# Kernel optimization log

Hardware: AMD Instinct MI355X
Metric: run time of the kernel (lower is better)

The kernel has to match this reference:

```python
import jax, jax.numpy as jnp
import numpy as np
import math

S, B, HID = 1024, 2, 2048
NH, KVH, HDIM = 16, 4, 128
FFN, E, TOPK = 4096, 8, 2
CAP_F = 1.0
Q_PER_KV = NH // KVH
GROUP = (Q_PER_KV + 2) * HDIM
QKV_SIZE = KVH * GROUP
T = S * B
CAPACITY = max(4, int(math.ceil(TOPK * CAP_F * T / E)))
EPS = 1.1920929e-07


def _xavier(key, shape, fan_in, fan_out):
    lim = math.sqrt(6.0 / (fan_in + fan_out))
    return jax.random.uniform(key, shape, jnp.float32, -lim, lim)


def setup_inputs() -> dict:
    key = jax.random.key(0)
    ks = jax.random.split(key, 8)
    return {
        'hidden_states': jax.random.normal(ks[0], (S, B, HID), jnp.float32),
        'ln1_w': jnp.ones((HID,), jnp.float32),
        'ln1_b': jnp.zeros((HID,), jnp.float32),
        'qkv_w': _xavier(ks[1], (QKV_SIZE, HID), HID, QKV_SIZE),
        'proj_w': _xavier(ks[2], (HID, NH * HDIM), NH * HDIM, HID),
        'ln2_w': jnp.ones((HID,), jnp.float32),
        'ln2_b': jnp.zeros((HID,), jnp.float32),
        'gate_w': _xavier(ks[3], (HID, E), HID, E),
        'w1': _xavier(ks[4], (E, HID, FFN), HID, FFN),  # expert fc1 [E, HID, FFN]
        'w2': _xavier(ks[5], (E, FFN, HID), FFN, HID),  # expert fc2 [E, FFN, HID]
    }


def _layer_norm(x, w, b):
    mu = x.mean(-1, keepdims=True)
    var = ((x - mu) ** 2).mean(-1, keepdims=True)
    return (x - mu) * jax.lax.rsqrt(var + 1e-5) * w + b


def _attention(hs, ln1_w, ln1_b, qkv_w, proj_w):
    ln1 = _layer_norm(hs, ln1_w, ln1_b)
    qkv = jnp.einsum('sbh,oh->sbo', ln1, qkv_w)
    qkv = qkv.reshape(S, B, KVH, GROUP)
    q_dim = Q_PER_KV * HDIM
    q = qkv[..., :q_dim].reshape(S, B, NH, HDIM)
    k = qkv[..., q_dim:q_dim + HDIM]          # [S,B,KVH,HDIM]
    v = qkv[..., q_dim + HDIM:]               # [S,B,KVH,HDIM]
    # batch-first, GQA expand kv heads
    q_bf = q.transpose(1, 0, 2, 3)                         # [B,S,NH,HDIM]
    k_bf = jnp.repeat(k.transpose(1, 0, 2, 3), Q_PER_KV, axis=2)
    v_bf = jnp.repeat(v.transpose(1, 0, 2, 3), Q_PER_KV, axis=2)
    scale = 1.0 / math.sqrt(HDIM)
    scores = jnp.einsum('bqhd,bkhd->bhqk', q_bf, k_bf) * scale
    causal = jnp.tril(jnp.ones((S, S), bool))
    scores = jnp.where(causal, scores, jnp.finfo(scores.dtype).min)
    attn = jax.nn.softmax(scores, axis=-1)
    out = jnp.einsum('bhqk,bkhd->bqhd', attn, v_bf)        # [B,S,NH,HDIM]
    out_sp = out.transpose(1, 0, 2, 3).reshape(S, B, NH * HDIM)
    return jnp.einsum('sbo,ho->sbh', out_sp, proj_w)


def _moe(x, gate_w, w1, w2):
    # x: [T, HID]; deterministic DeepSpeed-style top-2 gating with capacity drop
    logits = jnp.einsum('th,he->te', x, gate_w)
    gates = jax.nn.softmax(logits, axis=-1)
    idx1 = jnp.argmax(gates, axis=-1)
    mask1 = jax.nn.one_hot(idx1, E, dtype=jnp.int32)
    logits2 = jnp.where(mask1.astype(bool), jnp.finfo(logits.dtype).min, logits)
    idx2 = jnp.argmax(logits2, axis=-1)
    mask2 = jax.nn.one_hot(idx2, E, dtype=jnp.int32)
    loc1 = jnp.cumsum(mask1, axis=0) - mask1                 # position within expert
    loc2 = jnp.cumsum(mask2, axis=0) - mask2 + mask1.sum(axis=0, keepdims=True)
    mask1 = mask1 * (loc1 < CAPACITY)
    mask2 = mask2 * (loc2 < CAPACITY)
    m1f = mask1.astype(gates.dtype)
    m2f = mask2.astype(gates.dtype)
    g1 = (gates * m1f).sum(-1)
    g2 = (gates * m2f).sum(-1)
    denom = jnp.maximum(g1 + g2, EPS)
    g1, g2 = g1 / denom, g2 / denom
    p1 = (loc1 * mask1).sum(-1)
    p2 = (loc2 * mask2).sum(-1)
    c1 = (g1[:, None] * m1f)[:, :, None] * jax.nn.one_hot(p1, CAPACITY, dtype=gates.dtype)[:, None, :]
    c2 = (g2[:, None] * m2f)[:, :, None] * jax.nn.one_hot(p2, CAPACITY, dtype=gates.dtype)[:, None, :]
    combine = c1 + c2                                        # [T,E,C]
    dispatch = (combine > 0).astype(x.dtype)
    xe = jnp.einsum('tec,th->ech', dispatch, x)              # [E,C,HID]
    h = jax.nn.gelu(jnp.einsum('ech,ehf->ecf', xe, w1), approximate=False)
    eo = jnp.einsum('ecf,efh->ech', h, w2)                   # [E,C,HID]
    return jnp.einsum('tec,ech->th', combine, eo)


def reference(hidden_states, ln1_w, ln1_b, qkv_w, proj_w, ln2_w, ln2_b, gate_w, w1, w2):
    h1 = hidden_states + _attention(hidden_states, ln1_w, ln1_b, qkv_w, proj_w)
    ln2 = _layer_norm(h1, ln2_w, ln2_b)
    moe_out = _moe(ln2.reshape(T, HID), gate_w, w1, w2).reshape(S, B, HID)
    return h1 + moe_out
```

## Files before the change

### kernel.cpp

```cpp
#include <hip/hip_runtime.h>
#include <math.h>

#define S_LEN 1024
#define BATCH 2
#define HIDN  2048
#define NHEAD 16
#define KVHN  4
#define HDIM  128
#define FFND  4096
#define NEXP  8
#define CAPC  512
#define TTOK  2048
#define QKVSZ 3072
#define GRP   768

#define BM  128
#define BKS 32
#define BKM 64
#define LDT 40

typedef float           f32x4 __attribute__((ext_vector_type(4)));
typedef __bf16          bf16x8 __attribute__((ext_vector_type(8)));
typedef unsigned short  u16x8 __attribute__((ext_vector_type(8)));
typedef unsigned short  u16x4 __attribute__((ext_vector_type(4)));

static __device__ __forceinline__ unsigned short f2bf(float f) {
  unsigned int u = __builtin_bit_cast(unsigned int, f);
  u += 0x7FFFu + ((u >> 16) & 1u);
  return (unsigned short)(u >> 16);
}
static __device__ __forceinline__ float bf2f(unsigned short h) {
  unsigned int u = ((unsigned int)h) << 16;
  return __builtin_bit_cast(float, u);
}
static __device__ __forceinline__ bf16x8 ldbf8(const unsigned short* p) {
  return __builtin_bit_cast(bf16x8, *(const u16x8*)p);
}
static __device__ __forceinline__ f32x4 mfma16(bf16x8 a, bf16x8 b, f32x4 c) {
  return __builtin_amdgcn_mfma_f32_16x16x32_bf16(a, b, c, 0, 0, 0);
}
static __device__ __forceinline__ void gl_lds16(const unsigned short* g, unsigned short* l) {
  __builtin_amdgcn_global_load_lds(
      (const __attribute__((address_space(1))) unsigned int*)g,
      (__attribute__((address_space(3))) unsigned int*)l, 16, 0, 0);
}

__global__ __launch_bounds__(256) void ln_kernel(
    const float* __restrict__ X, const float* __restrict__ W, const float* __restrict__ Bi,
    unsigned short* __restrict__ Yh, unsigned short* __restrict__ Yl, float* __restrict__ Yf) {
  __shared__ float red[256];
  int t = blockIdx.x, tid = threadIdx.x;
  const float* row = X + (size_t)t * HIDN;
  float x[8];
  {
    float4 a = *(const float4*)(row + tid * 8);
    float4 b = *(const float4*)(row + tid * 8 + 4);
    x[0]=a.x; x[1]=a.y; x[2]=a.z; x[3]=a.w; x[4]=b.x; x[5]=b.y; x[6]=b.z; x[7]=b.w;
  }
  float s = 0.f;
#pragma unroll
  for (int j = 0; j < 8; j++) s += x[j];
  red[tid] = s; __syncthreads();
  for (int o = 128; o > 0; o >>= 1) { if (tid < o) red[tid] += red[tid + o]; __syncthreads(); }
  float mu = red[0] * (1.0f / HIDN);
  __syncthreads();
  float ss = 0.f;
#pragma unroll
  for (int j = 0; j < 8; j++) { float d = x[j] - mu; ss += d * d; }
  red[tid] = ss; __syncthreads();
  for (int o = 128; o > 0; o >>= 1) { if (tid < o) red[tid] += red[tid + o]; __syncthreads(); }
  float var = red[0] * (1.0f / HIDN);
  float rstd = 1.0f / sqrtf(var + 1e-5f);
#pragma unroll
  for (int j = 0; j < 8; j++) {
    int hh = tid * 8 + j;
    float y = (x[j] - mu) * rstd * W[hh] + Bi[hh];
    size_t idx = (size_t)t * HIDN + hh;
    if (Yf) Yf[idx] = y;
    unsigned short hv = f2bf(y);
    Yh[idx] = hv;
    if (Yl) Yl[idx] = f2bf(y - bf2f(hv));
  }
}

__global__ __launch_bounds__(256) void wsplit(const float* __restrict__ W,
    unsigned short* __restrict__ Wh, unsigned short* __restrict__ Wl) {
  size_t i = ((size_t)blockIdx.x * 256 + threadIdx.x) * 8;
  float4 a = *(const float4*)(W + i);
  float4 b = *(const float4*)(W + i + 4);
  float v[8] = {a.x, a.y, a.z, a.w, b.x, b.y, b.z, b.w};
  u16x8 hv, lv;
#pragma unroll
  for (int j = 0; j < 8; j++) {
    unsigned short h = f2bf(v[j]);
    hv[j] = h; lv[j] = f2bf(v[j] - bf2f(h));
  }
  *(u16x8*)(Wh + i) = hv;
  *(u16x8*)(Wl + i) = lv;
}

__global__ __launch_bounds__(256) void tconv(const float* __restrict__ W,
    unsigned short* __restrict__ Wt, int K, int N) {
  __shared__ unsigned short T[64][72];
  int z = blockIdx.z;
  const float* Wz = W + (size_t)z * K * N;
  unsigned short* Oz = Wt + (size_t)z * N * K;
  int k0 = blockIdx.y * 64, n0 = blockIdx.x * 64;
  int tid = threadIdx.x;
  int kr = (tid >> 4) << 1, n4 = (tid & 15) << 2;
#pragma unroll
  for (int i = 0; i < 2; i++) {
    int k = kr + i * 32;
    float4 a = *(const float4*)(Wz + (size_t)(k0 + k) * N + n0 + n4);
    float4 b = *(const float4*)(Wz + (size_t)(k0 + k + 1) * N + n0 + n4);
    float av[4] = {a.x, a.y, a.z, a.w};
    float bv[4] = {b.x, b.y, b.z, b.w};
#pragma unroll
    for (int j = 0; j < 4; j++) {
      unsigned int pk = (unsigned int)f2bf(av[j]) | ((unsigned int)f2bf(bv[j]) << 16);
      *(unsigned int*)&T[n4 + j][k] = pk;
    }
  }
  __syncthreads();
  int nr = tid >> 3, c = (tid & 7) << 3;
#pragma unroll
  for (int r = 0; r < 2; r++) {
    int n = nr + r * 32;
    u16x8 v = *(const u16x8*)&T[n][c];
    *(u16x8*)(Oz + (size_t)(n0 + n) * K + k0 + c) = v;
  }
}

__global__ __launch_bounds__(256) void gemm_x3s(
    const unsigned short* __restrict__ Ah, const unsigned short* __restrict__ Al,
    const unsigned short* __restrict__ Bh, const unsigned short* __restrict__ Bl,
    float* __restrict__ Cp, int M, int N, int K2, int ldk) {
  __shared__ __align__(16) unsigned short sAh[2][4096], sAl[2][4096], sBh[2][4096], sBl[2][4096];
  int tid = threadIdx.x;
  int nbm = M >> 7, nbn = N >> 7, per = nbm * nbn;
  int cpx = gridDim.x >> 3;
  int bid = blockIdx.x;
  int l = (bid & 7) * cpx + (bid >> 3);
  int kh = l / per;
  int r = l % per;
  int nb = r / nbm, mb = r % nbm;
  int m0 = mb * BM, n0 = nb * BM;
  size_t ko = (size_t)kh * K2;
  int wv = tid >> 6, lane = tid & 63;
  int wr = wv >> 1, wc = wv & 1;
  int lm = lane & 15, lk = lane >> 4;
  f32x4 acc[4][4];
#pragma unroll
  for (int mi = 0; mi < 4; mi++)
#pragma unroll
    for (int ni = 0; ni < 4; ni++) { acc[mi][ni][0]=0.f; acc[mi][ni][1]=0.f; acc[mi][ni][2]=0.f; acc[mi][ni][3]=0.f; }
  int ri = lane >> 2, ccx = lane & 3;
  int swze = (ccx ^ (ri & 3)) * 8;
  int g0 = wv * 2, g1 = g0 + 1;
  const unsigned short* pah0 = Ah + (size_t)(m0 + g0 * 16 + ri) * ldk + ko + swze;
  const unsigned short* pah1 = Ah + (size_t)(m0 + g1 * 16 + ri) * ldk + ko + swze;
  const unsigned short* pal0 = Al + (size_t)(m0 + g0 * 16 + ri) * ldk + ko + swze;
  const unsigned short* pal1 = Al + (size_t)(m0 + g1 * 16 + ri) * ldk + ko + swze;
  const unsigned short* pbh0 = Bh + (size_t)(n0 + g0 * 16 + ri) * ldk + ko + swze;
  const unsigned short* pbh1 = Bh + (size_t)(n0 + g1 * 16 + ri) * ldk + ko + swze;
  const unsigned short* pbl0 = Bl + (size_t)(n0 + g0 * 16 + ri) * ldk + ko + swze;
  const unsigned short* pbl1 = Bl + (size_t)(n0 + g1 * 16 + ri) * ldk + ko + swze;
  int d0 = g0 * 512, d1 = g1 * 512;
  auto stage = [&](int buf, int ks) {
    gl_lds16(pah0 + ks, &sAh[buf][d0]); gl_lds16(pah1 + ks, &sAh[buf][d1]);
    gl_lds16(pal0 + ks, &sAl[buf][d0]); gl_lds16(pal1 + ks, &sAl[buf][d1]);
    gl_lds16(pbh0 + ks, &sBh[buf][d0]); gl_lds16(pbh1 + ks, &sBh[buf][d1]);
    gl_lds16(pbl0 + ks, &sBl[buf][d0]); gl_lds16(pbl1 + ks, &sBl[buf][d1]);
  };
  int nt = K2 / BKS;
  stage(0, 0);
  stage(1, BKS);
  int sa = (lk ^ (lm & 3)) * 8;
  for (int t = 0; t < nt; t++) {
    if (t + 1 < nt) { asm volatile("s_waitcnt vmcnt(8)" ::: "memory"); }
    else            { asm volatile("s_waitcnt vmcnt(0)" ::: "memory"); }
    __builtin_amdgcn_sched_barrier(0);
    __builtin_amdgcn_s_barrier();
    int cur = t & 1;
    bf16x8 fah[4], fal[4], fbh[4], fbl[4];
#pragma unroll
    for (int mi = 0; mi < 4; mi++) {
      int ro = (wr * 64 + mi * 16 + lm) * 32 + sa;
      fah[mi] = ldbf8(&sAh[cur][ro]); fal[mi] = ldbf8(&sAl[cur][ro]);
    }
#pragma unroll
    for (int ni = 0; ni < 4; ni++) {
      int ro = (wc * 64 + ni * 16 + lm) * 32 + sa;
      fbh[ni] = ldbf8(&sBh[cur][ro]); fbl[ni] = ldbf8(&sBl[cur][ro]);
    }
#pragma unroll
    for (int mi = 0; mi < 4; mi++)
#pragma unroll
      for (int ni = 0; ni < 4; ni++) {
        acc[mi][ni] = mfma16(fah[mi], fbh[ni], acc[mi][ni]);
        acc[mi][ni] = mfma16(fal[mi], fbh[ni], acc[mi][ni]);
        acc[mi][ni] = mfma16(fah[mi], fbl[ni], acc[mi][ni]);
      }
    __builtin_amdgcn_s_barrier();
    if (t + 2 < nt) stage(cur, (t + 2) * BKS);
  }
  float* Cslab = Cp + (size_t)kh * M * N;
#pragma unroll
  for (int mi = 0; mi < 4; mi++)
#pragma unroll
    for (int ni = 0; ni < 4; ni++)
#pragma unroll
      for (int rr = 0; rr < 4; rr++) {
        int row = m0 + wr * 64 + mi * 16 + lk * 4 + rr;
        int col = n0 + wc * 64 + ni * 16 + lm;
        Cslab[(size_t)row * N + col] = acc[mi][ni][rr];
      }
}

template<int GELU, int SPLITK>
__global__ __launch_bounds__(256) void gemm_moe(
    const unsigned short* __restrict__ A, const unsigned short* __restrict__ Bt,
    void* __restrict__ Cp, int M, int N, int K, int ld) {
  __shared__ __align__(16) unsigned short sA[2][8192], sB[2][8192];
  int tid = threadIdx.x;
  int nbm = M >> 7, nbn = N >> 7, per = nbm * nbn;
  int cpx = gridDim.x >> 3;
  int bid = blockIdx.x;
  int l = (bid & 7) * cpx + (bid >> 3);
  int z = l / per;
  int r = l % per;
  int nb = r / nbm, mb = r % nbm;
  int m0 = mb * BM, n0 = nb * BM;
  const unsigned short* Az;
  const unsigned short* Bz;
  if (SPLITK) {
    int e = z >> 1, kh = z & 1;
    Az = A + (size_t)e * M * ld + (size_t)kh * K;
    Bz = Bt + (size_t)e * N * ld + (size_t)kh * K;
  } else {
    Az = A + (size_t)z * M * ld;
    Bz = Bt + (size_t)z * N * ld;
  }
  int wv = tid >> 6, lane = tid & 63;
  int wr = wv >> 1, wc = wv & 1;
  int lm = lane & 15, lk = lane >> 4;
  f32x4 acc[4][4];
#pragma unroll
  for (int mi = 0; mi < 4; mi++)
#pragma unroll
    for (int ni = 0; ni < 4; ni++) { acc[mi][ni][0]=0.f; acc[mi][ni][1]=0.f; acc[mi][ni][2]=0.f; acc[mi][ni][3]=0.f; }
  int ri = lane >> 3, cc8 = lane & 7;
  int swze = (cc8 ^ ri) * 8;
  const unsigned short* pa[4];
  const unsigned short* pb[4];
#pragma unroll
  for (int j = 0; j < 4; j++) {
    int g = wv * 4 + j;
    pa[j] = Az + (size_t)(m0 + g * 8 + ri) * ld + swze;
    pb[j] = Bz + (size_t)(n0 + g * 8 + ri) * ld + swze;
  }
  int dbase = wv * 4 * 512;
  auto stage = [&](int buf, int ks) {
#pragma unroll
    for (int j = 0; j < 4; j++) {
      gl_lds16(pa[j] + ks, &sA[buf][dbase + j * 512]);
      gl_lds16(pb[j] + ks, &sB[buf][dbase + j * 512]);
    }
  };
  int nt = K / BKM;
  stage(0, 0);
  stage(1, BKM);
  int sw = lm & 7;
  for (int t = 0; t < nt; t++) {
    if (t + 1 < nt) { asm volatile("s_waitcnt vmcnt(8)" ::: "memory"); }
    else            { asm volatile("s_waitcnt vmcnt(0)" ::: "memory"); }
    __builtin_amdgcn_sched_barrier(0);
    __builtin_amdgcn_s_barrier();
    int cur = t & 1;
#pragma unroll
    for (int h = 0; h < 2; h++) {
      int kc = lk + h * 4;
      int sa = ((kc ^ sw)) * 8;
      bf16x8 fa[4], fb[4];
#pragma unroll
      for (int mi = 0; mi < 4; mi++) fa[mi] = ldbf8(&sA[cur][(wr * 64 + mi * 16 + lm) * 64 + sa]);
#pragma unroll
      for (int ni = 0; ni < 4; ni++) fb[ni] = ldbf8(&sB[cur][(wc * 64 + ni * 16 + lm) * 64 + sa]);
#pragma unroll
      for (int mi = 0; mi < 4; mi++)
#pragma unroll
        for (int ni = 0; ni < 4; ni++)
          acc[mi][ni] = mfma16(fa[mi], fb[ni], acc[mi][ni]);
    }
    __builtin_amdgcn_s_barrier();
    if (t + 2 < nt) stage(cur, (t + 2) * BKM);
  }
#pragma unroll
  for (int mi = 0; mi < 4; mi++)
#pragma unroll
    for (int ni = 0; ni < 4; ni++)
#pragma unroll
      for (int rr = 0; rr < 4; rr++) {
        int row = m0 + wr * 64 + mi * 16 + lk * 4 + rr;
        int col = n0 + wc * 64 + ni * 16 + lm;
        size_t idx = (size_t)z * M * N + (size_t)row * N + col;
        float v = acc[mi][ni][rr];
        if (GELU) {
          float gv = 0.5f * v * (1.0f + erff(v * 0.70710678118654752f));
          ((unsigned short*)Cp)[idx] = f2bf(gv);
        } else {
          ((float*)Cp)[idx] = v;
        }
      }
}

__global__ __launch_bounds__(256) void h1comb(
    const float* __restrict__ hs, const float* __restrict__ p, float* __restrict__ h1) {
  size_t i = ((size_t)blockIdx.x * 256 + threadIdx.x) * 8;
  const float* p0 = p + i;
  const float* p1 = p + (size_t)TTOK * HIDN + i;
#pragma unroll
  for (int j = 0; j < 8; j += 4) {
    float4 a = *(const float4*)(hs + i + j);
    float4 b = *(const float4*)(p0 + j);
    float4 c = *(const float4*)(p1 + j);
    float4 o;
    o.x = a.x + b.x + c.x; o.y = a.y + b.y + c.y;
    o.z = a.z + b.z + c.z; o.w = a.w + b.w + c.w;
    *(float4*)(h1 + i + j) = o;
  }
}

__global__ __launch_bounds__(256) void repack_kernel(
    const float* __restrict__ qkvp,
    unsigned short* __restrict__ Qh, unsigned short* __restrict__ Ql,
    unsigned short* __restrict__ Kh, unsigned short* __restrict__ Kl,
    unsigned short* __restrict__ Vh, unsigned short* __restrict__ Vl) {
  int t = blockIdx.x; int s = t / BATCH, b = t % BATCH;
  const float* row0 = qkvp + (size_t)t * QKVSZ;
  const float* row1 = row0 + (size_t)TTOK * QKVSZ;
  int tid = threadIdx.x;
  for (int idx = tid; idx < 2048; idx += 256) {
    int hh = idx >> 7, d = idx & 127;
    int o_in = (hh >> 2) * GRP + (hh & 3) * 128 + d;
    float val = row0[o_in] + row1[o_in];
    unsigned short hv = f2bf(val), lv = f2bf(val - bf2f(hv));
    size_t o = ((size_t)(b * NHEAD + hh) * S_LEN + s) * HDIM + d;
    Qh[o] = hv; Ql[o] = lv;
  }
  for (int idx = tid; idx < 512; idx += 256) {
    int g = idx >> 7, d = idx & 127;
    int o_in = g * GRP + 512 + d;
    float val = row0[o_in] + row1[o_in];
    unsigned short hv = f2bf(val), lv = f2bf(val - bf2f(hv));
    size_t o = ((size_t)(b * KVHN + g) * S_LEN + s) * HDIM + d;
    Kh[o] = hv; Kl[o] = lv;
  }
  for (int idx = tid; idx < 512; idx += 256) {
    int g = idx >> 7, d = idx & 127;
    int o_in = g * GRP + 640 + d;
    float val = row0[o_in] + row1[o_in];
    unsigned short hv = f2bf(val), lv = f2bf(val - bf2f(hv));
    size_t o = ((size_t)(b * KVHN + g) * HDIM + d) * S_LEN + s;
    Vh[o] = hv; Vl[o] = lv;
  }
}

__global__ __launch_bounds__(256) void attn4(
    const unsigned short* __restrict__ Qh, const unsigned short* __restrict__ Ql,
    const unsigned short* __restrict__ Kh, const unsigned short* __restrict__ Kl,
    const unsigned short* __restrict__ Vh, const unsigned short* __restrict__ Vl,
    unsigned short* __restrict__ Oh, unsigned short* __restrict__ Ol) {
  __shared__ __align__(16) unsigned short sK[2][2][32 * 128];
  __shared__ __align__(16) unsigned short Ph[4][2][16 * LDT], Pl[4][2][16 * LDT];
  int qt = blockIdx.x, g = blockIdx.y, b = blockIdx.z;
  int tid = threadIdx.x, wv = tid >> 6, lane = tid & 63;
  int lm = lane & 15, lk = lane >> 4;
  int hh = g * 4 + wv;
  int q0 = qt * 16;
  const float scale = 0.08838834764831845f;
  int r0 = wv * 4 + (lane >> 4);
  int c16 = lane & 15;
  int dsw = (c16 * 8) ^ ((r0 & 7) << 3);
  const unsigned short* kbh = Kh + (size_t)((b * KVHN + g) * S_LEN) * HDIM;
  const unsigned short* kbl = Kl + (size_t)((b * KVHN + g) * S_LEN) * HDIM;
  auto stageK = [&](int buf, int k0) {
    unsigned short* dh = &sK[buf][0][0];
    unsigned short* dl = &sK[buf][1][0];
    gl_lds16(kbh + (size_t)(k0 + r0) * HDIM + dsw,      dh + wv * 512);
    gl_lds16(kbh + (size_t)(k0 + r0 + 16) * HDIM + dsw, dh + 2048 + wv * 512);
    gl_lds16(kbl + (size_t)(k0 + r0) * HDIM + dsw,      dl + wv * 512);
    gl_lds16(kbl + (size_t)(k0 + r0 + 16) * HDIM + dsw, dl + 2048 + wv * 512);
  };
  bf16x8 qfh[4], qfl[4];
  {
    size_t qb = ((size_t)(b * NHEAD + hh) * S_LEN + q0 + lm) * HDIM + lk * 8;
#pragma unroll
    for (int dc = 0; dc < 4; dc++) {
      qfh[dc] = ldbf8(Qh + qb + dc * 32);
      qfl[dc] = ldbf8(Ql + qb + dc * 32);
    }
  }
  f32x4 accO[8];
#pragma unroll
  for (int dt = 0; dt < 8; dt++) { accO[dt][0]=0.f; accO[dt][1]=0.f; accO[dt][2]=0.f; accO[dt][3]=0.f; }
  float mrun = -3.4e38f, lrun = 0.f;
  int nch = (q0 + 47) >> 5;
  stageK(0, 0);
  asm volatile("s_waitcnt vmcnt(0)" ::: "memory");
  __syncthreads();
  int cur = 0;
  for (int ck = 0; ck < nch; ck++) {
    int k0 = ck * 32;
    if (ck + 1 < nch) stageK(cur ^ 1, k0 + 32);
    f32x4 sc[2];
    sc[0][0]=0.f; sc[0][1]=0.f; sc[0][2]=0.f; sc[0][3]=0.f;
    sc[1][0]=0.f; sc[1][1]=0.f; sc[1][2]=0.f; sc[1][3]=0.f;
#pragma unroll
    for (int t2 = 0; t2 < 2; t2++) {
      int row = t2 * 16 + lm;
#pragma unroll
      for (int dc = 0; dc < 4; dc++) {
        int ce = (dc * 32 + lk * 8) ^ ((row & 7) << 3);
        bf16x8 kfh = ldbf8(&sK[cur][0][row * 128 + ce]);
        bf16x8 kfl = ldbf8(&sK[cur][1][row * 128 + ce]);
        sc[t2] = mfma16(kfh, qfh[dc], sc[t2]);
        sc[t2] = mfma16(kfl, qfh[dc], sc[t2]);
        sc[t2] = mfma16(kfh, qfl[dc], sc[t2]);
      }
    }
    float pv[8];
    float pmax = -3.4e38f;
#pragma unroll
    for (int t2 = 0; t2 < 2; t2++)
#pragma unroll
      for (int rr = 0; rr < 4; rr++) {
        int key = k0 + t2 * 16 + lk * 4 + rr;
        float sv = sc[t2][rr] * scale;
        if (key > q0 + lm) sv = -3.4e38f;
        pv[t2 * 4 + rr] = sv;
        pmax = fmaxf(pmax, sv);
      }
    pmax = fmaxf(pmax, __shfl_xor(pmax, 16));
    pmax = fmaxf(pmax, __shfl_xor(pmax, 32));
    float mnew = fmaxf(mrun, pmax);
    float fsc = expf(mrun - mnew);
    float psum = 0.f;
#pragma unroll
    for (int j = 0; j < 8; j++) { pv[j] = expf(pv[j] - mnew); psum += pv[j]; }
    psum = psum + __shfl_xor(psum, 16);
    psum = psum + __shfl_xor(psum, 32);
    lrun = lrun * fsc + psum;
#pragma unroll
    for (int dt = 0; dt < 8; dt++)
#pragma unroll
      for (int rr = 0; rr < 4; rr++) accO[dt][rr] *= fsc;
    int pb = ck & 1;
#pragma unroll
    for (int t2 = 0; t2 < 2; t2++) {
      u16x4 wh, wl;
#pragma unroll
      for (int rr = 0; rr < 4; rr++) {
        float p = pv[t2 * 4 + rr];
        unsigned short hv = f2bf(p);
        wh[rr] = hv; wl[rr] = f2bf(p - bf2f(hv));
      }
      int ad = lm * LDT + t2 * 16 + lk * 4;
      *(u16x4*)&Ph[wv][pb][ad] = wh;
      *(u16x4*)&Pl[wv][pb][ad] = wl;
    }
    bf16x8 pfh = ldbf8(&Ph[wv][pb][lm * LDT + lk * 8]);
    bf16x8 pfl = ldbf8(&Pl[wv][pb][lm * LDT + lk * 8]);
#pragma unroll
    for (int dt = 0; dt < 8; dt++) {
      size_t vo = ((size_t)((b * KVHN + g) * HDIM + dt * 16 + lm)) * S_LEN + k0 + lk * 8;
      bf16x8 vfh = ldbf8(Vh + vo);
      bf16x8 vfl = ldbf8(Vl + vo);
      accO[dt] = mfma16(vfh, pfh, accO[dt]);
      accO[dt] = mfma16(vfl, pfh, accO[dt]);
      accO[dt] = mfma16(vfh, pfl, accO[dt]);
    }
    mrun = mnew;
    asm volatile("s_waitcnt vmcnt(0)" ::: "memory");
    __syncthreads();
    cur ^= 1;
  }
  float inv = 1.0f / lrun;
#pragma unroll
  for (int dt = 0; dt < 8; dt++)
#pragma unroll
    for (int rr = 0; rr < 4; rr++) {
      float o = accO[dt][rr] * inv;
      int d = dt * 16 + lk * 4 + rr;
      int srow = q0 + lm;
      size_t idx = ((size_t)(srow * BATCH + b)) * HIDN + hh * HDIM + d;
      unsigned short hv = f2bf(o);
      Oh[idx] = hv; Ol[idx] = f2bf(o - bf2f(hv));
    }
}

__global__ __launch_bounds__(256) void gate_logits_kernel(
    const float* __restrict__ X, const float* __restrict__ GW, float* __restrict__ L) {
  __shared__ float red[256][8];
  int t = blockIdx.x, tid = threadIdx.x;
  const float* x = X + (size_t)t * HIDN + tid * 8;
  float acc[8] = {0.f,0.f,0.f,0.f,0.f,0.f,0.f,0.f};
#pragma unroll
  for (int j = 0; j < 8; j++) {
    float xv = x[j];
    const float* gp = GW + (size_t)(tid * 8 + j) * NEXP;
    float4 g0 = *(const float4*)gp;
    float4 g1 = *(const float4*)(gp + 4);
    acc[0] += xv * g0.x; acc[1] += xv * g0.y; acc[2] += xv * g0.z; acc[3] += xv * g0.w;
    acc[4] += xv * g1.x; acc[5] += xv * g1.y; acc[6] += xv * g1.z; acc[7] += xv * g1.w;
  }
#pragma unroll
  for (int k = 0; k < 8; k++) red[tid][k] = acc[k];
  __syncthreads();
  for (int o = 128; o > 0; o >>= 1) {
    if (tid < o) {
#pragma unroll
      for (int k = 0; k < 8; k++) red[tid][k] += red[tid + o][k];
    }
    __syncthreads();
  }
  if (tid < 8) L[(size_t)t * NEXP + tid] = red[0][tid];
}

__global__ __launch_bounds__(1024) void routing_kernel(
    const float* __restrict__ L, int* __restrict__ slot_token,
    int* __restrict__ tE1, int* __restrict__ tP1, float* __restrict__ tG1,
    int* __restrict__ tE2, int* __restrict__ tP2, float* __restrict__ tG2) {
  __shared__ unsigned int sc[1024][8];
  __shared__ unsigned int stot[8];
  int i = threadIdx.x;
  for (int j = i; j < NEXP * CAPC; j += 1024) slot_token[j] = -1;

  int e1[2], e2[2]; float g1[2], g2[2];
  unsigned int v[8] = {0,0,0,0,0,0,0,0};
#pragma unroll
  for (int u = 0; u < 2; u++) {
    int t = 2 * i + u;
    float l[8];
    float m = -3.4e38f;
#pragma unroll
    for (int e = 0; e < 8; e++) { l[e] = L[(size_t)t * NEXP + e]; m = fmaxf(m, l[e]); }
    float ex[8]; float se = 0.f;
#pragma unroll
    for (int e = 0; e < 8; e++) { ex[e] = expf(l[e] - m); se += ex[e]; }
    int b1 = 0; float bv = l[0];
    for (int e = 1; e < 8; e++) if (l[e] > bv) { bv = l[e]; b1 = e; }
    int b2 = -1; float bv2 = 0.f;
    for (int e = 0; e < 8; e++) {
      if (e == b1) continue;
      if (b2 < 0 || l[e] > bv2) { b2 = e; bv2 = l[e]; }
    }
    e1[u] = b1; e2[u] = b2;
    g1[u] = ex[b1] / se; g2[u] = ex[b2] / se;
    v[b1 >> 1] += 1u << ((b1 & 1) * 16);
    v[4 + (b2 >> 1)] += 1u << ((b2 & 1) * 16);
  }
  unsigned int cur[8];
#pragma unroll
  for (int k = 0; k < 8; k++) cur[k] = v[k];
  for (int off = 1; off < 1024; off <<= 1) {
#pragma unroll
    for (int k = 0; k < 8; k++) sc[i][k] = cur[k];
    __syncthreads();
    if (i >= off) {
#pragma unroll
      for (int k = 0; k < 8; k++) cur[k] += sc[i - off][k];
    }
    __syncthreads();
  }
  if (i == 1023) {
#pragma unroll
    for (int k = 0; k < 8; k++) stot[k] = cur[k];
  }
  __syncthreads();
  unsigned int excl[8];
#pragma unroll
  for (int k = 0; k < 8; k++) excl[k] = cur[k] - v[k];

#pragma unroll
  for (int u = 0; u < 2; u++) {
    int t = 2 * i + u;
    int a1 = e1[u], a2 = e2[u];
    int loc1 = (int)((excl[a1 >> 1] >> ((a1 & 1) * 16)) & 0xFFFFu);
    int loc2 = (int)((excl[4 + (a2 >> 1)] >> ((a2 & 1) * 16)) & 0xFFFFu);
    if (u == 1) {
      if (a1 == e1[0]) loc1 += 1;
      if (a2 == e2[0]) loc2 += 1;
    }
    loc2 += (int)((stot[a2 >> 1] >> ((a2 & 1) * 16)) & 0xFFFFu);
    bool k1 = loc1 < CAPC, k2 = loc2 < CAPC;
    float G1 = k1 ? g1[u] : 0.f, G2 = k2 ? g2[u] : 0.f;
    float den = fmaxf(G1 + G2, 1.1920929e-07f);
    G1 /= den; G2 /= den;
    tE1[t] = a1; tP1[t] = k1 ? loc1 : 0; tG1[t] = G1;
    tE2[t] = a2; tP2[t] = k2 ? loc2 : 0; tG2[t] = G2;
    if (k1) slot_token[a1 * CAPC + loc1] = t;
    if (k2) slot_token[a2 * CAPC + loc2] = t;
  }
}

__global__ __launch_bounds__(256) void gather_kernel(
    const int* __restrict__ slot_token, const unsigned short* __restrict__ Xb,
    unsigned short* __restrict__ XE) {
  int slot = blockIdx.x;
  int t = slot_token[slot];
  unsigned short* dst = XE + (size_t)slot * HIDN + threadIdx.x * 8;
  if (t >= 0) {
    *(u16x8*)dst = *(const u16x8*)(Xb + (size_t)t * HIDN + threadIdx.x * 8);
  } else {
    u16x8 zz = {0,0,0,0,0,0,0,0};
    *(u16x8*)dst = zz;
  }
}

__global__ __launch_bounds__(256) void combine_kernel(
    const float* __restrict__ h1, const float* __restrict__ eo2,
    const int* __restrict__ tE1, const int* __restrict__ tP1, const float* __restrict__ tG1,
    const int* __restrict__ tE2, const int* __restrict__ tP2, const float* __restrict__ tG2,
    float* __restrict__ outp) {
  int t = blockIdx.x, tid = threadIdx.x;
  float G1 = tG1[t], G2 = tG2[t];
  size_t MN = (size_t)CAPC * HIDN;
  size_t b1 = ((size_t)tE1[t] * 2) * MN + (size_t)tP1[t] * HIDN;
  size_t b2 = ((size_t)tE2[t] * 2) * MN + (size_t)tP2[t] * HIDN;
  size_t rowo = (size_t)t * HIDN;
  int c = tid * 8;
#pragma unroll
  for (int j = 0; j < 8; j += 4) {
    float4 hv  = *(const float4*)(h1 + rowo + c + j);
    float4 e1a = *(const float4*)(eo2 + b1 + c + j);
    float4 e1b = *(const float4*)(eo2 + b1 + MN + c + j);
    float4 e2a = *(const float4*)(eo2 + b2 + c + j);
    float4 e2b = *(const float4*)(eo2 + b2 + MN + c + j);
    float4 o;
    o.x = hv.x + G1 * (e1a.x + e1b.x) + G2 * (e2a.x + e2b.x);
    o.y = hv.y + G1 * (e1a.y + e1b.y) + G2 * (e2a.y + e2b.y);
    o.z = hv.z + G1 * (e1a.z + e1b.z) + G2 * (e2a.z + e2b.z);
    o.w = hv.w + G1 * (e1a.w + e1b.w) + G2 * (e2a.w + e2b.w);
    *(float4*)(outp + rowo + c + j) = o;
  }
}

extern "C" void kernel_launch(void* const* d_in, const int* in_sizes, int n_in,
                              void* d_out, int out_size, void* d_ws, size_t ws_size,
                              hipStream_t stream) {
  const float* hs    = (const float*)d_in[0];
  const float* ln1w  = (const float*)d_in[1];
  const float* ln1b  = (const float*)d_in[2];
  const float* qkvw  = (const float*)d_in[3];
  const float* projw = (const float*)d_in[4];
  const float* ln2w  = (const float*)d_in[5];
  const float* ln2b  = (const float*)d_in[6];
  const float* gatew = (const float*)d_in[7];
  const float* w1    = (const float*)d_in[8];
  const float* w2    = (const float*)d_in[9];
  float* outp = (float*)d_out;

  char* base = (char*)d_ws;
  size_t off = 0;
  auto alloc = [&](size_t bytes) -> void* {
    void* r = base + off;
    off = (off + bytes + 255) & ~(size_t)255;
    return r;
  };
  unsigned short* ln1h = (unsigned short*)alloc((size_t)TTOK * HIDN * 2);
  unsigned short* ln1l = (unsigned short*)alloc((size_t)TTOK * HIDN * 2);
  float* qkvp = (float*)alloc((size_t)2 * TTOK * QKVSZ * 4);
  unsigned short* Qh = (unsigned short*)alloc((size_t)BATCH * NHEAD * S_LEN * HDIM * 2);
  unsigned short* Ql = (unsigned short*)alloc((size_t)BATCH * NHEAD * S_LEN * HDIM * 2);
  unsigned short* Kh = (unsigned short*)alloc((size_t)BATCH * KVHN * S_LEN * HDIM * 2);
  unsigned short* Kl = (unsigned short*)alloc((size_t)BATCH * KVHN * S_LEN * HDIM * 2);
  unsigned short* Vh = (unsigned short*)alloc((size_t)BATCH * KVHN * S_LEN * HDIM * 2);
  unsigned short* Vl = (unsigned short*)alloc((size_t)BATCH * KVHN * S_LEN * HDIM * 2);
  unsigned short* oh = (unsigned short*)alloc((size_t)TTOK * HIDN * 2);
  unsigned short* ol = (unsigned short*)alloc((size_t)TTOK * HIDN * 2);
  float* h1p = (float*)alloc((size_t)2 * TTOK * HIDN * 4);
  float* h1 = (float*)alloc((size_t)TTOK * HIDN * 4);
  float* xf = (float*)alloc((size_t)TTOK * HIDN * 4);
  unsigned short* xb = (unsigned short*)alloc((size_t)TTOK * HIDN * 2);
  float* logits = (float*)alloc((size_t)TTOK * NEXP * 4);
  int* slot = (int*)alloc((size_t)NEXP * CAPC * 4);
  int* tE1 = (int*)alloc((size_t)TTOK * 4);
  int* tP1 = (int*)alloc((size_t)TTOK * 4);
  int* tE2 = (int*)alloc((size_t)TTOK * 4);
  int* tP2 = (int*)alloc((size_t)TTOK * 4);
  float* tG1 = (float*)alloc((size_t)TTOK * 4);
  float* tG2 = (float*)alloc((size_t)TTOK * 4);
  unsigned short* xe = (unsigned short*)alloc((size_t)NEXP * CAPC * HIDN * 2);
  unsigned short* hmid = (unsigned short*)alloc((size_t)NEXP * CAPC * FFND * 2);
  float* eo2 = (float*)alloc((size_t)NEXP * 2 * CAPC * HIDN * 4);
  unsigned short* qwh = (unsigned short*)alloc((size_t)QKVSZ * HIDN * 2);
  unsigned short* qwl = (unsigned short*)alloc((size_t)QKVSZ * HIDN * 2);
  unsigned short* pwh = (unsigned short*)alloc((size_t)HIDN * HIDN * 2);
  unsigned short* pwl = (unsigned short*)alloc((size_t)HIDN * HIDN * 2);
  unsigned short* wt = (unsigned short*)alloc((size_t)NEXP * FFND * HIDN * 2);
  (void)ws_size; (void)in_sizes; (void)n_in; (void)out_size;

  ln_kernel<<<TTOK, 256, 0, stream>>>(hs, ln1w, ln1b, ln1h, ln1l, nullptr);
  wsplit<<<(QKVSZ * HIDN) / 2048, 256, 0, stream>>>(qkvw, qwh, qwl);
  wsplit<<<(HIDN * HIDN) / 2048, 256, 0, stream>>>(projw, pwh, pwl);
  gemm_x3s<<<dim3((QKVSZ / BM) * (TTOK / BM) * 2), 256, 0, stream>>>(
      ln1h, ln1l, qwh, qwl, qkvp, TTOK, QKVSZ, HIDN / 2, HIDN);
  repack_kernel<<<TTOK, 256, 0, stream>>>(qkvp, Qh, Ql, Kh, Kl, Vh, Vl);
  attn4<<<dim3(S_LEN / 16, KVHN, BATCH), 256, 0, stream>>>(Qh, Ql, Kh, Kl, Vh, Vl, oh, ol);
  gemm_x3s<<<dim3((HIDN / BM) * (TTOK / BM) * 2), 256, 0, stream>>>(
      oh, ol, pwh, pwl, h1p, TTOK, HIDN, HIDN / 2, HIDN);
  h1comb<<<(TTOK * HIDN) / 2048, 256, 0, stream>>>(hs, h1p, h1);
  ln_kernel<<<TTOK, 256, 0, stream>>>(h1, ln2w, ln2b, xb, nullptr, xf);
  gate_logits_kernel<<<TTOK, 256, 0, stream>>>(xf, gatew, logits);
  routing_kernel<<<1, 1024, 0, stream>>>(logits, slot, tE1, tP1, tG1, tE2, tP2, tG2);
  gather_kernel<<<NEXP * CAPC, 256, 0, stream>>>(slot, xb, xe);
  tconv<<<dim3(FFND / 64, HIDN / 64, NEXP), 256, 0, stream>>>(w1, wt, HIDN, FFND);
  gemm_moe<1, 0><<<dim3((FFND / BM) * (CAPC / BM) * NEXP), 256, 0, stream>>>(
      xe, wt, (void*)hmid, CAPC, FFND, HIDN, HIDN);
  tconv<<<dim3(HIDN / 64, FFND / 64, NEXP), 256, 0, stream>>>(w2, wt, FFND, HIDN);
  gemm_moe<0, 1><<<dim3((HIDN / BM) * (CAPC / BM) * NEXP * 2), 256, 0, stream>>>(
      hmid, wt, (void*)eo2, CAPC, HIDN, FFND / 2, FFND);
  combine_kernel<<<TTOK, 256, 0, stream>>>(h1, eo2, tE1, tP1, tG1, tE2, tP2, tG2, outp);
}
```

Measured before the change: 791.7 us.

## Enlarge MoE GEMM tiles to 256x256 with 512 threads and 4-stage pipeline

Replaces the 128x128, 256-thread MoE expert GEMM with a 256x256 tile run by 8 waves, each computing a 128x64 sub-tile. The K step drops to 32 and the LDS ring grows to 4 stages, with vmcnt waits stepped down near the end of the loop. It also raises wave priority around the MFMA block. The aim is more data reuse per load and deeper latency hiding, at the cost of more registers per thread (32 accumulator fragments), 64KB of LDS, and far fewer blocks in the grid, which may leave the GPU underfilled.

```diff
diff --git a/kernel.cpp b/kernel.cpp
--- a/kernel.cpp
+++ b/kernel.cpp
@@ -16,7 +16,6 @@
 
 #define BM  128
 #define BKS 32
-#define BKM 64
 #define LDT 40
 
 typedef float           f32x4 __attribute__((ext_vector_type(4)));
@@ -218,19 +217,19 @@
 }
 
 template<int GELU, int SPLITK>
-__global__ __launch_bounds__(256) void gemm_moe(
+__global__ __launch_bounds__(512, 2) void gemm_moe256(
     const unsigned short* __restrict__ A, const unsigned short* __restrict__ Bt,
     void* __restrict__ Cp, int M, int N, int K, int ld) {
-  __shared__ __align__(16) unsigned short sA[2][8192], sB[2][8192];
+  __shared__ __align__(16) unsigned short sA[4][8192], sB[4][8192];
   int tid = threadIdx.x;
-  int nbm = M >> 7, nbn = N >> 7, per = nbm * nbn;
+  int nbm = M >> 8, nbn = N >> 8, per = nbm * nbn;
   int cpx = gridDim.x >> 3;
   int bid = blockIdx.x;
   int l = (bid & 7) * cpx + (bid >> 3);
   int z = l / per;
   int r = l % per;
   int nb = r / nbm, mb = r % nbm;
-  int m0 = mb * BM, n0 = nb * BM;
+  int m0 = mb * 256, n0 = nb * 256;
   const unsigned short* Az;
   const unsigned short* Bz;
   if (SPLITK) {
@@ -241,68 +240,67 @@
     Az = A + (size_t)z * M * ld;
     Bz = Bt + (size_t)z * N * ld;
   }
-  int wv = tid >> 6, lane = tid & 63;
-  int wr = wv >> 1, wc = wv & 1;
+  int wid = tid >> 6, lane = tid & 63;
+  int wm = wid >> 2, wn = wid & 3;
   int lm = lane & 15, lk = lane >> 4;
-  f32x4 acc[4][4];
-#pragma unroll
-  for (int mi = 0; mi < 4; mi++)
+  f32x4 acc[8][4];
+#pragma unroll
+  for (int mi = 0; mi < 8; mi++)
 #pragma unroll
     for (int ni = 0; ni < 4; ni++) { acc[mi][ni][0]=0.f; acc[mi][ni][1]=0.f; acc[mi][ni][2]=0.f; acc[mi][ni][3]=0.f; }
-  int ri = lane >> 3, cc8 = lane & 7;
-  int swze = (cc8 ^ ri) * 8;
-  const unsigned short* pa[4];
-  const unsigned short* pb[4];
-#pragma unroll
-  for (int j = 0; j < 4; j++) {
-    int g = wv * 4 + j;
-    pa[j] = Az + (size_t)(m0 + g * 8 + ri) * ld + swze;
-    pb[j] = Bz + (size_t)(n0 + g * 8 + ri) * ld + swze;
-  }
-  int dbase = wv * 4 * 512;
-  auto stage = [&](int buf, int ks) {
-#pragma unroll
-    for (int j = 0; j < 4; j++) {
-      gl_lds16(pa[j] + ks, &sA[buf][dbase + j * 512]);
-      gl_lds16(pb[j] + ks, &sB[buf][dbase + j * 512]);
-    }
+  int li0 = tid, li1 = 512 + tid;
+  int ra0 = li0 >> 2, ca0 = li0 & 3;
+  int ra1 = li1 >> 2, ca1 = li1 & 3;
+  const unsigned short* pA0 = Az + (size_t)(m0 + ra0) * ld + (ca0 ^ (ra0 & 3)) * 8;
+  const unsigned short* pA1 = Az + (size_t)(m0 + ra1) * ld + (ca1 ^ (ra1 & 3)) * 8;
+  const unsigned short* pB0 = Bz + (size_t)(n0 + ra0) * ld + (ca0 ^ (ra0 & 3)) * 8;
+  const unsigned short* pB1 = Bz + (size_t)(n0 + ra1) * ld + (ca1 ^ (ra1 & 3)) * 8;
+  int dj0 = wid * 512;
+  int dj1 = 4096 + wid * 512;
+  auto stage = [&](int slot, int ks) {
+    gl_lds16(pA0 + ks, &sA[slot][dj0]);
+    gl_lds16(pA1 + ks, &sA[slot][dj1]);
+    gl_lds16(pB0 + ks, &sB[slot][dj0]);
+    gl_lds16(pB1 + ks, &sB[slot][dj1]);
   };
-  int nt = K / BKM;
-  stage(0, 0);
-  stage(1, BKM);
-  int sw = lm & 7;
-  for (int t = 0; t < nt; t++) {
-    if (t + 1 < nt) { asm volatile("s_waitcnt vmcnt(8)" ::: "memory"); }
-    else            { asm volatile("s_waitcnt vmcnt(0)" ::: "memory"); }
+  int ns = K >> 5;
+  stage(0, 0); stage(1, 32); stage(2, 64); stage(3, 96);
+  int sa = (lk ^ (lm & 3)) * 8;
+  for (int s = 0; s < ns; s++) {
+    int rem = ns - 1 - s; if (rem > 3) rem = 3;
+    if (rem == 3)      { asm volatile("s_waitcnt vmcnt(12)" ::: "memory"); }
+    else if (rem == 2) { asm volatile("s_waitcnt vmcnt(8)"  ::: "memory"); }
+    else if (rem == 1) { asm volatile("s_waitcnt vmcnt(4)"  ::: "memory"); }
+    else               { asm volatile("s_waitcnt vmcnt(0)"  ::: "memory"); }
     __builtin_amdgcn_sched_barrier(0);
     __builtin_amdgcn_s_barrier();
-    int cur = t & 1;
-#pragma unroll
-    for (int h = 0; h < 2; h++) {
-      int kc = lk + h * 4;
-      int sa = ((kc ^ sw)) * 8;
-      bf16x8 fa[4], fb[4];
-#pragma unroll
-      for (int mi = 0; mi < 4; mi++) fa[mi] = ldbf8(&sA[cur][(wr * 64 + mi * 16 + lm) * 64 + sa]);
-#pragma unroll
-      for (int ni = 0; ni < 4; ni++) fb[ni] = ldbf8(&sB[cur][(wc * 64 + ni * 16 + lm) * 64 + sa]);
-#pragma unroll
-      for (int mi = 0; mi < 4; mi++)
-#pragma unroll
-        for (int ni = 0; ni < 4; ni++)
-          acc[mi][ni] = mfma16(fa[mi], fb[ni], acc[mi][ni]);
-    }
+    int slot = s & 3;
+    bf16x8 fb[4];
+#pragma unroll
+    for (int ni = 0; ni < 4; ni++)
+      fb[ni] = ldbf8(&sB[slot][(wn * 64 + ni * 16 + lm) * 32 + sa]);
+    bf16x8 fa[8];
+#pragma unroll
+    for (int mi = 0; mi < 8; mi++)
+      fa[mi] = ldbf8(&sA[slot][(wm * 128 + mi * 16 + lm) * 32 + sa]);
+    __builtin_amdgcn_s_setprio(1);
+#pragma unroll
+    for (int mi = 0; mi < 8; mi++)
+#pragma unroll
+      for (int ni = 0; ni < 4; ni++)
+        acc[mi][ni] = mfma16(fa[mi], fb[ni], acc[mi][ni]);
+    __builtin_amdgcn_s_setprio(0);
     __builtin_amdgcn_s_barrier();
-    if (t + 2 < nt) stage(cur, (t + 2) * BKM);
-  }
-#pragma unroll
-  for (int mi = 0; mi < 4; mi++)
+    if (s + 4 < ns) stage(slot, (s + 4) * 32);
+  }
+#pragma unroll
+  for (int mi = 0; mi < 8; mi++)
 #pragma unroll
     for (int ni = 0; ni < 4; ni++)
 #pragma unroll
       for (int rr = 0; rr < 4; rr++) {
-        int row = m0 + wr * 64 + mi * 16 + lk * 4 + rr;
-        int col = n0 + wc * 64 + ni * 16 + lm;
+        int row = m0 + wm * 128 + mi * 16 + lk * 4 + rr;
+        int col = n0 + wn * 64 + ni * 16 + lm;
         size_t idx = (size_t)z * M * N + (size_t)row * N + col;
         float v = acc[mi][ni][rr];
         if (GELU) {
@@ -716,10 +714,10 @@
   routing_kernel<<<1, 1024, 0, stream>>>(logits, slot, tE1, tP1, tG1, tE2, tP2, tG2);
   gather_kernel<<<NEXP * CAPC, 256, 0, stream>>>(slot, xb, xe);
   tconv<<<dim3(FFND / 64, HIDN / 64, NEXP), 256, 0, stream>>>(w1, wt, HIDN, FFND);
-  gemm_moe<1, 0><<<dim3((FFND / BM) * (CAPC / BM) * NEXP), 256, 0, stream>>>(
+  gemm_moe256<1, 0><<<dim3(NEXP * (CAPC / 256) * (FFND / 256)), 512, 0, stream>>>(
       xe, wt, (void*)hmid, CAPC, FFND, HIDN, HIDN);
   tconv<<<dim3(HIDN / 64, FFND / 64, NEXP), 256, 0, stream>>>(w2, wt, FFND, HIDN);
-  gemm_moe<0, 1><<<dim3((HIDN / BM) * (CAPC / BM) * NEXP * 2), 256, 0, stream>>>(
+  gemm_moe256<0, 1><<<dim3(NEXP * 2 * (CAPC / 256) * (HIDN / 256)), 512, 0, stream>>>(
       hmid, wt, (void*)eo2, CAPC, HIDN, FFND / 2, FFND);
   combine_kernel<<<TTOK, 256, 0, stream>>>(h1, eo2, tE1, tP1, tG1, tE2, tP2, tG2, outp);
 }
```

Result: slower. 875.1 us (+10.5%).
